# Optimization experiments

Measured on AMD Instinct MI355X. Metric: run time of the kernel, lower is better.

The kernel has to match this reference:

```python
import jax, jax.numpy as jnp
import numpy as np

NUM_TOKENS = 8192
TOKEN_DIM = 256
N = 65536
TOPK = 5
DECAY = 0.1      # cur_decay (set_decay_updates never called -> stays at init decay)
EPS = 1e-5
TEMP = 1.0


def setup_inputs() -> dict:
    key = jax.random.key(0)
    k1, k2 = jax.random.split(key)
    return {
        "inputs_flatten": jax.random.normal(k1, (N, TOKEN_DIM), dtype=jnp.float32),
        "embed": jax.random.normal(k2, (NUM_TOKENS, TOKEN_DIM), dtype=jnp.float32),
        "cluster_size": jnp.zeros((NUM_TOKENS,), dtype=jnp.float32),
        "cluster_sum": jnp.zeros((NUM_TOKENS,), dtype=jnp.float32),
        "embed_avg": jnp.zeros((NUM_TOKENS, TOKEN_DIM), dtype=jnp.float32),
    }


def reference(inputs_flatten, embed, cluster_size, cluster_sum, embed_avg):
    x = inputs_flatten                              # [N, D]
    # squared euclidean distances to codebook: [N, K]
    distances = (jnp.sum(x * x, axis=1, keepdims=True)
                 + jnp.sum(embed * embed, axis=1)
                 - 2.0 * (x @ embed.T))
    # top-k nearest codes (smallest distance)
    neg_topk, topk_idx = jax.lax.top_k(-distances, TOPK)   # [N, k]
    topk_dist = -neg_topk
    weights = jax.nn.softmax(-topk_dist / TEMP, axis=1)    # [N, k]
    # scatter soft weights into dense one-hot-ish encodings [N, K]
    rows = jnp.arange(x.shape[0])[:, None]
    encodings = jnp.zeros_like(distances).at[rows, topk_idx].set(weights)
    encoding_indices = jnp.argmax(encodings, axis=1)[:, None]   # [N, 1]

    # training-mode EMA codebook update (module default is training=True)
    encoding_sum = jnp.sum(encodings, axis=0)                   # [K]
    new_cluster_sum = cluster_sum + encoding_sum
    new_cluster_size = cluster_size * DECAY + encoding_sum * (1.0 - DECAY)
    embed_sum = encodings.T @ x                                 # [K, D]
    new_embed_avg = embed_avg * DECAY + embed_sum * (1.0 - DECAY)
    smoothed = (new_cluster_size + EPS) / (jnp.sum(new_cluster_size) + NUM_TOKENS * EPS)
    cs = smoothed * jnp.sum(new_cluster_size)
    new_embed = new_embed_avg / cs[:, None]                     # embed.data.copy_(...)

    quantize = encodings @ new_embed                            # [N, D]
    quantize = jax.lax.stop_gradient(quantize - x) + x          # straight-through
    return quantize, encoding_indices
```

## Files before the change

kernel.cpp:

```cpp
#include <hip/hip_runtime.h>
#include <hip/hip_bf16.h>
#include <math.h>
#include <limits.h>

#define NROWS 65536
#define DIM   256
#define NCODE 8192
#define NTOPK 5

typedef __attribute__((ext_vector_type(4))) float     f32x4;
typedef __attribute__((ext_vector_type(4))) int       i32x4;
typedef __attribute__((ext_vector_type(4))) unsigned  u32x4;

#define WS_ESWZ   0u
#define WS_CINIT  2097152u
#define WS_CAND   2129920u
#define WS_ENTR   2129920u
#define WS_IDX5   10518528u
#define WS_W5     11829248u
#define WS_ENCSUM 13139968u
#define WS_CNT    13172736u
#define WS_OFFS   13205504u
#define WS_CURS   13238272u
#define WS_SFAC   13271040u
#define WS_NEWEMB 13271296u

#define ENT_PER_BLK 64
#define NENT (NROWS * NTOPK)

__device__ __forceinline__ void gl_lds16(const void* g, void* l) {
  __builtin_amdgcn_global_load_lds(
      (const __attribute__((address_space(1))) unsigned int*)g,
      (__attribute__((address_space(3))) unsigned int*)l, 16, 0, 0);
}

__device__ __forceinline__ unsigned f2key(float f) {
  unsigned u = __float_as_uint(f);
  return (u & 0x80000000u) ? ~u : (u | 0x80000000u);
}
__device__ __forceinline__ float key2f(unsigned k) {
  unsigned u = (k & 0x80000000u) ? (k ^ 0x80000000u) : ~k;
  return __uint_as_float(u);
}

__global__ __launch_bounds__(256) void k_prep(const float* __restrict__ embed,
                                              signed char* __restrict__ eswz,
                                              int* __restrict__ cinit) {
  const int code = blockIdx.x;
  const int d = threadIdx.x;
  float v = embed[code * DIM + d];
  float qf = fminf(127.f, fmaxf(-127.f, rintf(16.f * v)));
  int q = (int)qf;
  __shared__ unsigned char rb[256];
  __shared__ int red[4];
  rb[d] = (unsigned char)(q & 255);
  int e2 = q * q;
  #pragma unroll
  for (int off = 32; off; off >>= 1) e2 += __shfl_down(e2, off);
  const int lane = d & 63, w = d >> 6;
  if (lane == 0) red[w] = e2;
  __syncthreads();
  if (d == 0) {
    int s = red[0] + red[1] + red[2] + red[3];
    cinit[code] = -(s >> 1) * 8192 + code;
  }
  if (d < 64) {
    unsigned u = (unsigned)rb[4 * d] | ((unsigned)rb[4 * d + 1] << 8) |
                 ((unsigned)rb[4 * d + 2] << 16) | ((unsigned)rb[4 * d + 3] << 24);
    const int cs = (d >> 2) ^ (code & 15);
    ((unsigned*)(eswz + code * 256))[(cs << 2) | (d & 3)] = u;
  }
}


struct PList { int a, b, c, d; };

__device__ __forceinline__ void ladder(PList& P, int t) {
  int c0 = min(P.a, t); P.a = max(P.a, t);
  int c1 = min(P.b, c0); P.b = max(P.b, c0);
  int c2 = min(P.c, c1); P.c = max(P.c, c1);
  P.d = max(P.d, c2);
}

__device__ __forceinline__ void psel(PList& P, i32x4 acc, i32x4 en) {
  int p0 = acc[0] * 8192 + en[0];
  int p1 = acc[1] * 8192 + en[1];
  int p2 = acc[2] * 8192 + en[2];
  int p3 = acc[3] * 8192 + en[3];
  int h1 = max(p0, p1);
  int h2 = max(p2, p3);
  int t1 = max(h1, h2);
  if (__any(t1 > P.d)) {
    int l1 = min(p0, p1), l2 = min(p2, p3);
    int t2 = max(min(h1, h2), max(l1, l2));
    ladder(P, t1);
    if (__any(t2 > P.d)) ladder(P, t2);
  }
}

__device__ __forceinline__ int pk4(f32x4 v) {
  int r = 0;
  #pragma unroll
  for (int j = 0; j < 4; ++j) {
    float q = fminf(127.f, fmaxf(-127.f, rintf(16.f * v[j])));
    r |= ((int)q & 255) << (8 * j);
  }
  return r;
}

__global__ __launch_bounds__(256, 4) void k_gemm(const float* __restrict__ x,
                                                 const signed char* __restrict__ eswz,
                                                 const int* __restrict__ cinit,
                                                 int* __restrict__ candk) {
  __shared__ signed char ebuf[3][8192];
  const int tid = threadIdx.x;
  const int lane = tid & 63, wave = tid >> 6;
  const int q = lane >> 4, ln = lane & 15;
  const int half = blockIdx.x & 1, rb = blockIdx.x >> 1;
  const int wrow0 = rb * 128 + wave * 32;
  const signed char* esw_h = eswz + (unsigned)half * (4096u * 256u);
  const int* cin_h = cinit + half * 4096;

  gl_lds16(esw_h + tid * 16, &ebuf[0][tid * 16]);
  gl_lds16(esw_h + 4096 + tid * 16, &ebuf[0][4096 + tid * 16]);

  i32x4 enc0 = *(const i32x4*)(cin_h + q * 4);
  i32x4 enc1 = *(const i32x4*)(cin_h + 16 + q * 4);

  i32x4 xf[2][4];
  #pragma unroll
  for (int t = 0; t < 2; ++t) {
    const float* xr = x + (unsigned)(wrow0 + t * 16 + ln) * DIM;
    #pragma unroll
    for (int s = 0; s < 4; ++s) {
      i32x4 dw;
      #pragma unroll
      for (int d = 0; d < 4; ++d)
        dw[d] = pk4(*(const f32x4*)(xr + s * 64 + q * 16 + d * 4));
      xf[t][s] = dw;
    }
  }

  PList P0 = {INT_MIN, INT_MIN, INT_MIN, INT_MIN};
  PList P1 = P0;

  int slot = 0;
  #pragma unroll 1
  for (int it = 0; it < 128; ++it) {
    const int nslot = (slot + 1 == 3) ? 0 : slot + 1;
    const int tl = (it < 127) ? it + 1 : 127;
    const signed char* src = esw_h + (unsigned)tl * 8192;
    gl_lds16(src + tid * 16, &ebuf[nslot][tid * 16]);
    gl_lds16(src + 4096 + tid * 16, &ebuf[nslot][4096 + tid * 16]);
    i32x4 enn0 = *(const i32x4*)(cin_h + tl * 32 + q * 4);
    i32x4 enn1 = *(const i32x4*)(cin_h + tl * 32 + 16 + q * 4);

    asm volatile("s_waitcnt vmcnt(4)\n\ts_barrier" ::: "memory");

    const signed char* eb = ebuf[slot];
    i32x4 a00 = {0, 0, 0, 0}, a01 = a00, a10 = a00, a11 = a00;
    __builtin_amdgcn_s_setprio(1);
    #pragma unroll
    for (int s = 0; s < 4; ++s) {
      const int chunk = (4 * s + q) ^ ln;
      i32x4 ea0 = *(const i32x4*)&eb[ln * 256 + chunk * 16];
      i32x4 ea1 = *(const i32x4*)&eb[4096 + ln * 256 + chunk * 16];
      a00 = __builtin_amdgcn_mfma_i32_16x16x64_i8(ea0, xf[0][s], a00, 0, 0, 0);
      a10 = __builtin_amdgcn_mfma_i32_16x16x64_i8(ea0, xf[1][s], a10, 0, 0, 0);
      a01 = __builtin_amdgcn_mfma_i32_16x16x64_i8(ea1, xf[0][s], a01, 0, 0, 0);
      a11 = __builtin_amdgcn_mfma_i32_16x16x64_i8(ea1, xf[1][s], a11, 0, 0, 0);
    }
    __builtin_amdgcn_s_setprio(0);
    psel(P0, a00, enc0);
    psel(P0, a01, enc1);
    psel(P1, a10, enc0);
    psel(P1, a11, enc1);

    enc0 = enn0; enc1 = enn1;
    slot = nslot;
  }

  {
    const int row0 = wrow0 + ln;
    i32x4 pk0 = {P0.a, P0.b, P0.c, P0.d};
    *(i32x4*)&candk[row0 * 32 + half * 16 + q * 4] = pk0;
    const int row1 = wrow0 + 16 + ln;
    i32x4 pk1 = {P1.a, P1.b, P1.c, P1.d};
    *(i32x4*)&candk[row1 * 32 + half * 16 + q * 4] = pk1;
  }
}

__global__ __launch_bounds__(256) void k_refine(const float* __restrict__ x,
                                                const float* __restrict__ embed,
                                                const int* __restrict__ candk,
                                                float* __restrict__ out_idx,
                                                int* __restrict__ idx5,
                                                float* __restrict__ w5,
                                                float* __restrict__ enc_sum,
                                                unsigned* __restrict__ cnt) {
  __shared__ float sh[4][8][66];
  const int wave = threadIdx.x >> 6, l = threadIdx.x & 63;
  const int row = blockIdx.x * 4 + wave;

  int k = candk[row * 32 + (l & 31)];
  int cd[8];
  #pragma unroll
  for (int j = 0; j < 8; ++j) {
    int m = k;
    #pragma unroll
    for (int off = 1; off < 32; off <<= 1) m = max(m, __shfl_xor(m, off));
    cd[j] = m & 8191;
    if (k == m) k = INT_MIN;
  }

  const float* xr = x + (unsigned)row * DIM;
  const f32x4 xv = *(const f32x4*)(xr + 4 * l);
  const float t0 = -2.f * xv[0], t1 = -2.f * xv[1];
  const float t2 = -2.f * xv[2], t3 = -2.f * xv[3];

  #pragma unroll
  for (int ci = 0; ci < 8; ++ci) {
    const f32x4 e = *(const f32x4*)(embed + (unsigned)cd[ci] * DIM + 4 * l);
    float p = e[0] * (e[0] + t0);
    p = fmaf(e[1], e[1] + t1, p);
    p = fmaf(e[2], e[2] + t2, p);
    p = fmaf(e[3], e[3] + t3, p);
    sh[wave][ci][l] = p;
  }
  asm volatile("s_waitcnt lgkmcnt(0)" ::: "memory");

  const int c = l >> 3, sub = l & 7;
  const float* sp = &sh[wave][c][sub * 8];
  f32x4 v0 = *(const f32x4*)sp;
  f32x4 v1 = *(const f32x4*)(sp + 4);
  double s64 = (double)v0[0] + (double)v0[1] + (double)v0[2] + (double)v0[3]
             + (double)v1[0] + (double)v1[1] + (double)v1[2] + (double)v1[3];
  s64 += __shfl_xor(s64, 1);
  s64 += __shfl_xor(s64, 2);
  s64 += __shfl_xor(s64, 4);

  double sc = __shfl(s64, (l & 7) * 8);
  unsigned fkey = f2key((float)sc);
  const int myc = cd[l & 7];

  bool used = false;
  int codes[5]; float svals[5];
  #pragma unroll
  for (int j = 0; j < 5; ++j) {
    unsigned kk = used ? 0xFFFFFFFFu : fkey;
    unsigned mm = kk;
    #pragma unroll
    for (int off = 1; off < 8; off <<= 1) mm = min(mm, (unsigned)__shfl_xor((int)mm, off));
    int cc = (kk == mm) ? myc : 0x7FFFFFFF;
    #pragma unroll
    for (int off = 1; off < 8; off <<= 1) cc = min(cc, __shfl_xor(cc, off));
    used = used || (myc == cc);
    codes[j] = cc;
    svals[j] = key2f(mm);
  }

  float ex[5], sum = 0.f;
  #pragma unroll
  for (int j = 0; j < 5; ++j) { ex[j] = expf(-(svals[j] - svals[0])); sum += ex[j]; }
  const float inv = 1.f / sum;

  if (l == 0) {
    out_idx[row] = (float)codes[0];
    #pragma unroll
    for (int j = 0; j < 5; ++j) {
      float w = ex[j] * inv;
      idx5[row * 5 + j] = codes[j];
      w5[row * 5 + j] = w;
      atomicAdd(&enc_sum[codes[j]], w);
      atomicAdd(&cnt[codes[j]], 1u);
    }
  }
}

__global__ __launch_bounds__(256) void k_scan(const unsigned* __restrict__ cnt,
                                              unsigned* __restrict__ offs,
                                              unsigned* __restrict__ cursor,
                                              const float* __restrict__ enc_sum,
                                              const float* __restrict__ cluster_size,
                                              float* __restrict__ sfac) {
  __shared__ unsigned part[256];
  __shared__ double sred[256];
  const int t = threadIdx.x;
  unsigned s = 0;
  for (int i = 0; i < 32; ++i) s += cnt[t * 32 + i];
  part[t] = s;
  double ds = 0.0;
  for (int i = t; i < NCODE; i += 256)
    ds += 0.1 * (double)cluster_size[i] + 0.9 * (double)enc_sum[i];
  sred[t] = ds;
  __syncthreads();
  if (t == 0) {
    unsigned run = 0;
    for (int i = 0; i < 256; ++i) { unsigned tmp = part[i]; part[i] = run; run += tmp; }
    double S = 0.0;
    for (int i = 0; i < 256; ++i) S += sred[i];
    sfac[0] = (float)(S / (S + (double)NCODE * 1e-5));
  }
  __syncthreads();
  unsigned off = part[t];
  for (int i = 0; i < 32; ++i) {
    unsigned c = cnt[t * 32 + i];
    offs[t * 32 + i] = off;
    cursor[t * 32 + i] = off;
    off += c;
  }
}

__global__ __launch_bounds__(256) void k_fill(const int* __restrict__ idx5,
                                              const float* __restrict__ w5,
                                              unsigned* __restrict__ cursor,
                                              uint2* __restrict__ entries) {
  const int i = blockIdx.x * 256 + threadIdx.x;
  if (i >= NENT) return;
  const unsigned c = (unsigned)idx5[i];
  const float w = w5[i];
  const unsigned row = (unsigned)i / 5u;
  const unsigned slot = atomicAdd(&cursor[c], 1u);
  entries[slot] = make_uint2((c << 16) | row, __float_as_uint(w));
}

__global__ __launch_bounds__(256) void k_accum2(const float* __restrict__ x,
                                                const uint2* __restrict__ entries,
                                                float* __restrict__ embsum) {
  __shared__ uint2 ent[ENT_PER_BLK];
  const int t = threadIdx.x;
  const unsigned base = blockIdx.x * ENT_PER_BLK;
  if (t < ENT_PER_BLK * 2)
    ((unsigned*)ent)[t] = ((const unsigned*)(entries + base))[t];
  __syncthreads();

  float acc = 0.f;
  unsigned cur = ent[0].x >> 16;
  #pragma unroll 8
  for (int i = 0; i < ENT_PER_BLK; ++i) {
    const uint2 e = ent[i];
    const unsigned code = e.x >> 16;
    const unsigned row = e.x & 0xFFFFu;
    const float w = __uint_as_float(e.y);
    if (code != cur) {
      atomicAdd(&embsum[cur * DIM + t], acc);
      acc = 0.f; cur = code;
    }
    acc = fmaf(w, x[row * DIM + t], acc);
  }
  atomicAdd(&embsum[cur * DIM + t], acc);
}

__global__ __launch_bounds__(256) void k_norm(const float* __restrict__ embed_avg,
                                              const float* __restrict__ cluster_size,
                                              const float* __restrict__ enc_sum,
                                              const float* __restrict__ sfac,
                                              float* __restrict__ embsum ) {
  const int k = blockIdx.x, d = threadIdx.x;
  const float ncs = 0.1f * cluster_size[k] + 0.9f * enc_sum[k];
  const float cs = (ncs + 1e-5f) * sfac[0];
  const unsigned o = (unsigned)k * DIM + d;
  embsum[o] = (0.1f * embed_avg[o] + 0.9f * embsum[o]) / cs;
}

__global__ __launch_bounds__(256) void k_quant(const int* __restrict__ idx5,
                                               const float* __restrict__ w5,
                                               const float* __restrict__ newemb,
                                               float* __restrict__ out) {
  const int d = threadIdx.x;
  const int rb = blockIdx.x * 16;
  #pragma unroll 2
  for (int r = 0; r < 16; ++r) {
    const int row = rb + r;
    float acc = 0.f;
    #pragma unroll
    for (int j = 0; j < 5; ++j)
      acc = fmaf(w5[row * 5 + j], newemb[(unsigned)idx5[row * 5 + j] * DIM + d], acc);
    out[(unsigned)row * DIM + d] = acc;
  }
}

extern "C" void kernel_launch(void* const* d_in, const int* in_sizes, int n_in,
                              void* d_out, int out_size, void* d_ws, size_t ws_size,
                              hipStream_t stream) {
  const float* x            = (const float*)d_in[0];
  const float* embed        = (const float*)d_in[1];
  const float* cluster_size = (const float*)d_in[2];
  const float* embed_avg    = (const float*)d_in[4];

  char* w = (char*)d_ws;
  signed char*    eswz   = (signed char*)(w + WS_ESWZ);
  int*            cinit  = (int*)(w + WS_CINIT);
  int*            candk  = (int*)(w + WS_CAND);
  int*            idx5   = (int*)(w + WS_IDX5);
  float*          w5     = (float*)(w + WS_W5);
  float*          encsum = (float*)(w + WS_ENCSUM);
  unsigned*       cnt    = (unsigned*)(w + WS_CNT);
  unsigned*       offs   = (unsigned*)(w + WS_OFFS);
  unsigned*       curs   = (unsigned*)(w + WS_CURS);
  float*          sfac   = (float*)(w + WS_SFAC);
  uint2*          entr   = (uint2*)(w + WS_ENTR);
  float*          embsum = (float*)(w + WS_NEWEMB);

  float* out_q   = (float*)d_out;
  float* out_idx = out_q + (size_t)NROWS * DIM;

  hipMemsetAsync(w + WS_ENCSUM, 0, 65536, stream);
  hipMemsetAsync(w + WS_NEWEMB, 0, (size_t)NCODE * DIM * 4, stream);

  k_prep<<<NCODE, 256, 0, stream>>>(embed, eswz, cinit);
  k_gemm<<<NROWS / 128 * 2, 256, 0, stream>>>(x, eswz, cinit, candk);
  k_refine<<<NROWS / 4, 256, 0, stream>>>(x, embed, candk, out_idx, idx5, w5, encsum, cnt);
  k_scan<<<1, 256, 0, stream>>>(cnt, offs, curs, encsum, cluster_size, sfac);
  k_fill<<<(NENT + 255) / 256, 256, 0, stream>>>(idx5, w5, curs, entr);
  k_accum2<<<NENT / ENT_PER_BLK, 256, 0, stream>>>(x, entr, embsum);
  k_norm<<<NCODE, 256, 0, stream>>>(embed_avg, cluster_size, encsum, sfac, embsum);
  k_quant<<<NROWS / 16, 256, 0, stream>>>(idx5, w5, embsum, out_q);
}
```

Measured before the change: 439.7 us.

## Split codebook GEMM into quarters with smaller tiles and deeper LDS ring

```diff
diff --git a/kernel.cpp b/kernel.cpp
--- a/kernel.cpp
+++ b/kernel.cpp
@@ -10,20 +10,19 @@
 
 typedef __attribute__((ext_vector_type(4))) float     f32x4;
 typedef __attribute__((ext_vector_type(4))) int       i32x4;
-typedef __attribute__((ext_vector_type(4))) unsigned  u32x4;
 
 #define WS_ESWZ   0u
 #define WS_CINIT  2097152u
-#define WS_CAND   2129920u
+#define WS_CANDK  2129920u
 #define WS_ENTR   2129920u
-#define WS_IDX5   10518528u
-#define WS_W5     11829248u
-#define WS_ENCSUM 13139968u
-#define WS_CNT    13172736u
-#define WS_OFFS   13205504u
-#define WS_CURS   13238272u
-#define WS_SFAC   13271040u
-#define WS_NEWEMB 13271296u
+#define WS_NEWEMB 6324224u
+#define WS_IDX5   18907136u
+#define WS_W5     20217856u
+#define WS_ENCSUM 21528576u
+#define WS_CNT    21561344u
+#define WS_OFFS   21594112u
+#define WS_CURS   21626880u
+#define WS_SFAC   21659648u
 
 #define ENT_PER_BLK 64
 #define NENT (NROWS * NTOPK)
@@ -108,24 +107,43 @@
   return r;
 }
 
-__global__ __launch_bounds__(256, 4) void k_gemm(const float* __restrict__ x,
+#define GBODY(IT, SL, NS)                                                      \
+  {                                                                            \
+    const int tl = ((IT) < 127) ? (IT) + 1 : 127;                              \
+    gl_lds16(esw_h + (unsigned)tl * 4096u + tid * 16, &ebuf[NS][tid * 16]);    \
+    i32x4 enn = *(const i32x4*)(cin_h + tl * 16 + q * 4);                      \
+    asm volatile("s_waitcnt vmcnt(2)\n\ts_barrier" ::: "memory");              \
+    const signed char* eb = ebuf[SL];                                          \
+    i32x4 a0 = {0, 0, 0, 0}, a1 = {0, 0, 0, 0};                                \
+    __builtin_amdgcn_s_setprio(1);                                             \
+    _Pragma("unroll")                                                          \
+    for (int s = 0; s < 4; ++s) {                                              \
+      const int chunk = (4 * s + q) ^ ln;                                      \
+      i32x4 ea = *(const i32x4*)&eb[ln * 256 + chunk * 16];                    \
+      a0 = __builtin_amdgcn_mfma_i32_16x16x64_i8(ea, xf[0][s], a0, 0, 0, 0);   \
+      a1 = __builtin_amdgcn_mfma_i32_16x16x64_i8(ea, xf[1][s], a1, 0, 0, 0);   \
+    }                                                                          \
+    __builtin_amdgcn_s_setprio(0);                                             \
+    psel(P0, a0, enc);                                                         \
+    psel(P1, a1, enc);                                                         \
+    enc = enn;                                                                 \
+  }
+
+__global__ __launch_bounds__(256, 8) void k_gemm(const float* __restrict__ x,
                                                  const signed char* __restrict__ eswz,
                                                  const int* __restrict__ cinit,
                                                  int* __restrict__ candk) {
-  __shared__ signed char ebuf[3][8192];
+  __shared__ signed char ebuf[4][4096];
   const int tid = threadIdx.x;
   const int lane = tid & 63, wave = tid >> 6;
   const int q = lane >> 4, ln = lane & 15;
-  const int half = blockIdx.x & 1, rb = blockIdx.x >> 1;
-  const int wrow0 = rb * 128 + wave * 32;
-  const signed char* esw_h = eswz + (unsigned)half * (4096u * 256u);
-  const int* cin_h = cinit + half * 4096;
+  const int quarter = blockIdx.x & 3, rblk = blockIdx.x >> 2;
+  const int wrow0 = rblk * 128 + wave * 32;
+  const signed char* esw_h = eswz + (unsigned)quarter * (2048u * 256u);
+  const int* cin_h = cinit + quarter * 2048;
 
   gl_lds16(esw_h + tid * 16, &ebuf[0][tid * 16]);
-  gl_lds16(esw_h + 4096 + tid * 16, &ebuf[0][4096 + tid * 16]);
-
-  i32x4 enc0 = *(const i32x4*)(cin_h + q * 4);
-  i32x4 enc1 = *(const i32x4*)(cin_h + 16 + q * 4);
+  i32x4 enc = *(const i32x4*)(cin_h + q * 4);
 
   i32x4 xf[2][4];
   #pragma unroll
@@ -144,49 +162,22 @@
   PList P0 = {INT_MIN, INT_MIN, INT_MIN, INT_MIN};
   PList P1 = P0;
 
-  int slot = 0;
   #pragma unroll 1
-  for (int it = 0; it < 128; ++it) {
-    const int nslot = (slot + 1 == 3) ? 0 : slot + 1;
-    const int tl = (it < 127) ? it + 1 : 127;
-    const signed char* src = esw_h + (unsigned)tl * 8192;
-    gl_lds16(src + tid * 16, &ebuf[nslot][tid * 16]);
-    gl_lds16(src + 4096 + tid * 16, &ebuf[nslot][4096 + tid * 16]);
-    i32x4 enn0 = *(const i32x4*)(cin_h + tl * 32 + q * 4);
-    i32x4 enn1 = *(const i32x4*)(cin_h + tl * 32 + 16 + q * 4);
-
-    asm volatile("s_waitcnt vmcnt(4)\n\ts_barrier" ::: "memory");
-
-    const signed char* eb = ebuf[slot];
-    i32x4 a00 = {0, 0, 0, 0}, a01 = a00, a10 = a00, a11 = a00;
-    __builtin_amdgcn_s_setprio(1);
-    #pragma unroll
-    for (int s = 0; s < 4; ++s) {
-      const int chunk = (4 * s + q) ^ ln;
-      i32x4 ea0 = *(const i32x4*)&eb[ln * 256 + chunk * 16];
-      i32x4 ea1 = *(const i32x4*)&eb[4096 + ln * 256 + chunk * 16];
-      a00 = __builtin_amdgcn_mfma_i32_16x16x64_i8(ea0, xf[0][s], a00, 0, 0, 0);
-      a10 = __builtin_amdgcn_mfma_i32_16x16x64_i8(ea0, xf[1][s], a10, 0, 0, 0);
-      a01 = __builtin_amdgcn_mfma_i32_16x16x64_i8(ea1, xf[0][s], a01, 0, 0, 0);
-      a11 = __builtin_amdgcn_mfma_i32_16x16x64_i8(ea1, xf[1][s], a11, 0, 0, 0);
-    }
-    __builtin_amdgcn_s_setprio(0);
-    psel(P0, a00, enc0);
-    psel(P0, a01, enc1);
-    psel(P1, a10, enc0);
-    psel(P1, a11, enc1);
-
-    enc0 = enn0; enc1 = enn1;
-    slot = nslot;
+  for (int ob = 0; ob < 32; ++ob) {
+    const int it0 = ob * 4;
+    GBODY(it0 + 0, 0, 1)
+    GBODY(it0 + 1, 1, 2)
+    GBODY(it0 + 2, 2, 3)
+    GBODY(it0 + 3, 3, 0)
   }
 
   {
     const int row0 = wrow0 + ln;
     i32x4 pk0 = {P0.a, P0.b, P0.c, P0.d};
-    *(i32x4*)&candk[row0 * 32 + half * 16 + q * 4] = pk0;
+    *(i32x4*)&candk[row0 * 64 + quarter * 16 + q * 4] = pk0;
     const int row1 = wrow0 + 16 + ln;
     i32x4 pk1 = {P1.a, P1.b, P1.c, P1.d};
-    *(i32x4*)&candk[row1 * 32 + half * 16 + q * 4] = pk1;
+    *(i32x4*)&candk[row1 * 64 + quarter * 16 + q * 4] = pk1;
   }
 }
 
@@ -202,13 +193,13 @@
   const int wave = threadIdx.x >> 6, l = threadIdx.x & 63;
   const int row = blockIdx.x * 4 + wave;
 
-  int k = candk[row * 32 + (l & 31)];
+  int k = candk[row * 64 + l];
   int cd[8];
   #pragma unroll
   for (int j = 0; j < 8; ++j) {
     int m = k;
     #pragma unroll
-    for (int off = 1; off < 32; off <<= 1) m = max(m, __shfl_xor(m, off));
+    for (int off = 1; off < 64; off <<= 1) m = max(m, __shfl_xor(m, off));
     cd[j] = m & 8191;
     if (k == m) k = INT_MIN;
   }
@@ -391,7 +382,7 @@
   char* w = (char*)d_ws;
   signed char*    eswz   = (signed char*)(w + WS_ESWZ);
   int*            cinit  = (int*)(w + WS_CINIT);
-  int*            candk  = (int*)(w + WS_CAND);
+  int*            candk  = (int*)(w + WS_CANDK);
   int*            idx5   = (int*)(w + WS_IDX5);
   float*          w5     = (float*)(w + WS_W5);
   float*          encsum = (float*)(w + WS_ENCSUM);
@@ -406,11 +397,11 @@
   float* out_idx = out_q + (size_t)NROWS * DIM;
 
   hipMemsetAsync(w + WS_ENCSUM, 0, 65536, stream);
+
+  k_prep<<<NCODE, 256, 0, stream>>>(embed, eswz, cinit);
+  k_gemm<<<NROWS / 128 * 4, 256, 0, stream>>>(x, eswz, cinit, candk);
+  k_refine<<<NROWS / 4, 256, 0, stream>>>(x, embed, candk, out_idx, idx5, w5, encsum, cnt);
   hipMemsetAsync(w + WS_NEWEMB, 0, (size_t)NCODE * DIM * 4, stream);
-
-  k_prep<<<NCODE, 256, 0, stream>>>(embed, eswz, cinit);
-  k_gemm<<<NROWS / 128 * 2, 256, 0, stream>>>(x, eswz, cinit, candk);
-  k_refine<<<NROWS / 4, 256, 0, stream>>>(x, embed, candk, out_idx, idx5, w5, encsum, cnt);
   k_scan<<<1, 256, 0, stream>>>(cnt, offs, curs, encsum, cluster_size, sfac);
   k_fill<<<(NENT + 255) / 256, 256, 0, stream>>>(idx5, w5, curs, entr);
   k_accum2<<<NENT / ENT_PER_BLK, 256, 0, stream>>>(x, entr, embsum);
```

Measured after the change: 756.4 us. 72.0% more time.
